# Optimization experiments

Hardware: AMD Instinct MI355X
Metric: run time of the kernel (lower is better)

The kernel has to match this reference:

```python
import jax, jax.numpy as jnp
import numpy as np

HEADS, MAX_SEQ, N_STATE = 8, 2048, 512
DEPTH = N_STATE // HEADS
B, S = 2, 2048
EPS = 1e-5


def setup_inputs() -> dict:
    key = jax.random.key(0)
    ks = jax.random.split(key, 8)
    sd = lambda f: 1.0 / np.sqrt(f)
    causal = jnp.tril(jnp.ones((S, S), dtype=bool))
    mask = jnp.where(causal, 0.0, -1e9).astype(jnp.float32)[None, None]
    return {
        "x": jax.random.normal(ks[0], (B, S, N_STATE), jnp.float32),
        "mask": mask,
        "W_qkv": jax.random.normal(ks[1], (N_STATE, 3 * N_STATE), jnp.float32) * sd(N_STATE),
        "b_qkv": jnp.zeros((3 * N_STATE,), jnp.float32),
        "W_proj": jax.random.normal(ks[2], (N_STATE, N_STATE), jnp.float32) * sd(N_STATE),
        "b_proj": jnp.zeros((N_STATE,), jnp.float32),
        "E": jax.random.normal(ks[3], (HEADS, MAX_SEQ, DEPTH), jnp.float32) * sd(DEPTH),
        "g1": jnp.ones((N_STATE,), jnp.float32),
        "be1": jnp.zeros((N_STATE,), jnp.float32),
        "g2": jnp.ones((N_STATE,), jnp.float32),
        "be2": jnp.zeros((N_STATE,), jnp.float32),
        "W_fc1": jax.random.normal(ks[4], (N_STATE, 4 * N_STATE), jnp.float32) * sd(N_STATE),
        "b_fc1": jnp.zeros((4 * N_STATE,), jnp.float32),
        "W_fc2": jax.random.normal(ks[5], (4 * N_STATE, N_STATE), jnp.float32) * sd(4 * N_STATE),
        "b_fc2": jnp.zeros((N_STATE,), jnp.float32),
    }


def _layernorm(x, g, b):
    mu = jnp.mean(x, axis=-1, keepdims=True)
    var = jnp.mean(jnp.square(x - mu), axis=-1, keepdims=True)
    return (x - mu) * jax.lax.rsqrt(var + EPS) * g + b


def _relative_skew(rel):
    # rel: [B, H, S, S] = q @ E_slice^T ; skew trick -> relative positions
    b, h, s, _ = rel.shape
    rel = jnp.pad(rel, ((0, 0), (0, 0), (0, 0), (1, 0)))  # [B,H,S,S+1]
    rel = rel.reshape(b, h, s + 1, s)
    return rel[:, :, 1:, :]  # [B,H,S,S]


def reference(x, mask, W_qkv, b_qkv, W_proj, b_proj, E, g1, be1, g2, be2,
              W_fc1, b_fc1, W_fc2, b_fc2):
    b, s, _ = x.shape
    a = _layernorm(x, g1, be1)
    qkv = a @ W_qkv + b_qkv  # [B,S,3N]
    q, k, v = jnp.split(qkv, 3, axis=-1)
    split = lambda t: t.reshape(b, s, HEADS, DEPTH).transpose(0, 2, 1, 3)  # [B,H,S,D]
    q, k, v = split(q), split(k), split(v)
    present = jnp.stack([k, v], axis=1)  # [B,2,H,S,D]

    w = jnp.einsum("bhqd,bhkd->bhqk", q, k)
    E_s = E[:, MAX_SEq if False else MAX_SEQ - s:, :]  # [H,S,D]
    rel = jnp.einsum("bhqd,hld->bhql", q, E_s)
    w = (w + _relative_skew(rel)) * (1.0 / np.sqrt(DEPTH))
    w = w + mask
    w = jax.nn.softmax(w, axis=-1)
    att = jnp.einsum("bhqk,bhkd->bhqd", w, v)
    att = att.transpose(0, 2, 1, 3).reshape(b, s, N_STATE)
    att = att @ W_proj + b_proj

    x = x + att
    m = _layernorm(x, g2, be2)
    m = jax.nn.gelu(m @ W_fc1 + b_fc1) @ W_fc2 + b_fc2
    x = x + m
    return (x, present)
```

## Files before the change

### kernel.cpp

```cpp
#include <hip/hip_runtime.h>
#include <stdint.h>

#define DEV __device__ __forceinline__

typedef __attribute__((ext_vector_type(8))) short bf16x8;
typedef __attribute__((ext_vector_type(4))) float f32x4;

DEV ushort f2bf(float f) {
  union { float f; uint32_t u; } c; c.f = f;
  return (ushort)((c.u + 0x7FFFu + ((c.u >> 16) & 1)) >> 16);
}

__global__ __launch_bounds__(256) void k_transpose_bf(const float* __restrict__ in,
                                                      ushort* __restrict__ out,
                                                      int R, int C) {
  __shared__ float t[32][33];
  int tx = threadIdx.x & 31, ty = threadIdx.x >> 5;
  int c0 = blockIdx.x * 32, r0 = blockIdx.y * 32;
#pragma unroll
  for (int k = 0; k < 4; ++k)
    t[ty + 8 * k][tx] = in[(size_t)(r0 + ty + 8 * k) * C + c0 + tx];
  __syncthreads();
#pragma unroll
  for (int k = 0; k < 4; ++k)
    out[(size_t)(c0 + ty + 8 * k) * R + r0 + tx] = f2bf(t[tx][ty + 8 * k]);
}

__global__ __launch_bounds__(256) void k_cvt_bf(const float* __restrict__ in,
                                                ushort* __restrict__ out, int n4) {
  int i = blockIdx.x * 256 + threadIdx.x;
  if (i >= n4) return;
  float4 v = reinterpret_cast<const float4*>(in)[i];
  ushort4 o; o.x = f2bf(v.x); o.y = f2bf(v.y); o.z = f2bf(v.z); o.w = f2bf(v.w);
  reinterpret_cast<ushort4*>(out)[i] = o;
}

__global__ __launch_bounds__(64) void k_ln(const float* __restrict__ x,
                                           const float* __restrict__ g,
                                           const float* __restrict__ be,
                                           ushort* __restrict__ out) {
  int row = blockIdx.x, lane = threadIdx.x;
  const float* xr = x + (size_t)row * 512 + lane * 8;
  float4 a = *reinterpret_cast<const float4*>(xr);
  float4 b = *reinterpret_cast<const float4*>(xr + 4);
  float xs[8] = {a.x, a.y, a.z, a.w, b.x, b.y, b.z, b.w};
  float s = 0.f, q = 0.f;
#pragma unroll
  for (int i = 0; i < 8; ++i) { s += xs[i]; q += xs[i] * xs[i]; }
#pragma unroll
  for (int off = 32; off; off >>= 1) { s += __shfl_xor(s, off); q += __shfl_xor(q, off); }
  float mu = s * (1.f / 512.f);
  float var = q * (1.f / 512.f) - mu * mu;
  float inv = rsqrtf(var + 1e-5f);
  const float* gp = g + lane * 8;
  const float* bp = be + lane * 8;
  ushort o[8];
#pragma unroll
  for (int i = 0; i < 8; ++i) o[i] = f2bf((xs[i] - mu) * inv * gp[i] + bp[i]);
  *reinterpret_cast<uint4*>(out + (size_t)row * 512 + lane * 8) = *reinterpret_cast<uint4*>(o);
}

template <int EPI>
__global__ __launch_bounds__(256) void k_gemm(
    const ushort* __restrict__ A, const ushort* __restrict__ Bt,
    int M, int N, int K,
    const float* __restrict__ bias, const float* __restrict__ res,
    float* __restrict__ outf, ushort* __restrict__ outb,
    float* __restrict__ present, ushort* __restrict__ qbf) {
  __shared__ ushort As[128][72];
  __shared__ ushort Bs[128][72];
  const int tid = threadIdx.x, lane = tid & 63, w = tid >> 6;
  const int g = lane >> 4, l16 = lane & 15;
  const int m0 = blockIdx.y * 128, n0 = blockIdx.x * 128;
  const int wm = (w >> 1) * 64, wn = (w & 1) * 64;
  f32x4 acc[4][4];
#pragma unroll
  for (int i = 0; i < 4; ++i)
#pragma unroll
    for (int j = 0; j < 4; ++j) acc[i][j] = (f32x4){0.f, 0.f, 0.f, 0.f};

  for (int k0 = 0; k0 < K; k0 += 64) {
#pragma unroll
    for (int c = 0; c < 4; ++c) {
      int cc = tid + 256 * c;
      int r = cc >> 3, k8 = (cc & 7) << 3;
      *reinterpret_cast<uint4*>(&As[r][k8]) =
          *reinterpret_cast<const uint4*>(&A[(size_t)(m0 + r) * K + k0 + k8]);
      *reinterpret_cast<uint4*>(&Bs[r][k8]) =
          *reinterpret_cast<const uint4*>(&Bt[(size_t)(n0 + r) * K + k0 + k8]);
    }
    __syncthreads();
#pragma unroll
    for (int kk = 0; kk < 2; ++kk) {
      bf16x8 af[4], bfr[4];
#pragma unroll
      for (int f = 0; f < 4; ++f) {
        af[f] = *reinterpret_cast<const bf16x8*>(&As[wm + f * 16 + l16][kk * 32 + g * 8]);
        bfr[f] = *reinterpret_cast<const bf16x8*>(&Bs[wn + f * 16 + l16][kk * 32 + g * 8]);
      }
#pragma unroll
      for (int i = 0; i < 4; ++i)
#pragma unroll
        for (int j = 0; j < 4; ++j)
          acc[i][j] = __builtin_amdgcn_mfma_f32_16x16x32_bf16(af[i], bfr[j], acc[i][j], 0, 0, 0);
    }
    __syncthreads();
  }

#pragma unroll
  for (int i = 0; i < 4; ++i)
#pragma unroll
    for (int j = 0; j < 4; ++j)
#pragma unroll
      for (int r = 0; r < 4; ++r) {
        int row = m0 + wm + i * 16 + g * 4 + r;
        int col = n0 + wn + j * 16 + l16;
        float v = acc[i][j][r] + bias[col];
        if constexpr (EPI == 0) {
          int third = col >> 9, hh = (col >> 6) & 7, d = col & 63;
          int bb = row >> 11, sq = row & 2047;
          if (third == 0) {
            qbf[((((size_t)bb * 8 + hh) * 2048) + sq) * 64 + d] = f2bf(v);
          } else {
            present[((((size_t)bb * 2 + (third - 1)) * 8 + hh) * 2048 + sq) * 64 + d] = v;
          }
        } else if constexpr (EPI == 1) {
          size_t idx = (size_t)row * N + col;
          outf[idx] = v + res[idx];
        } else {
          float u = 0.7978845608f * (v + 0.044715f * v * v * v);
          float e = __expf(2.f * u);
          float th = 1.f - 2.f / (e + 1.f);
          outb[(size_t)row * N + col] = f2bf(0.5f * v * (1.f + th));
        }
      }
}

__global__ __launch_bounds__(256) void k_attn(
    const ushort* __restrict__ qbf, const float* __restrict__ present,
    const ushort* __restrict__ Ebf, ushort* __restrict__ attb) {
  constexpr int S = 2048;
  __shared__ ushort Ks[64][72];
  __shared__ ushort Vt[64][72];
  __shared__ ushort Es[128][72];
  __shared__ float Rs[4][16][80];
  __shared__ ushort Ps[4][16][72];
  const int tid = threadIdx.x, lane = tid & 63, w = tid >> 6;
  const int g = lane >> 4, l16 = lane & 15;
  const int bh = blockIdx.y, b = bh >> 3, h = bh & 7;
  const float* kp = present + (((size_t)b * 2 + 0) * 8 + h) * S * 64;
  const float* vp = present + (((size_t)b * 2 + 1) * 8 + h) * S * 64;
  const ushort* qp = qbf + (size_t)bh * S * 64;
  const ushort* ep = Ebf + (size_t)h * S * 64;

  for (int half = 0; half < 2; ++half) {
    const int qt = half ? 31 - (int)blockIdx.x : (int)blockIdx.x;
    const int i0 = qt * 64;
    const int iw = i0 + w * 16;
    bf16x8 qf[2];
#pragma unroll
    for (int kk = 0; kk < 2; ++kk)
      qf[kk] = *reinterpret_cast<const bf16x8*>(&qp[(size_t)(iw + l16) * 64 + kk * 32 + g * 8]);
    f32x4 o[4];
#pragma unroll
    for (int fv = 0; fv < 4; ++fv) o[fv] = (f32x4){0.f, 0.f, 0.f, 0.f};
    float mrun[4], lrun[4];
#pragma unroll
    for (int r = 0; r < 4; ++r) { mrun[r] = -1e30f; lrun[r] = 0.f; }

    const int nkt = qt + 1;
    for (int kt = 0; kt < nkt; ++kt) {
      const int j0 = kt * 64;
#pragma unroll
      for (int c = 0; c < 4; ++c) {
        int cc = tid + 256 * c;
        int j = cc >> 4, d4 = (cc & 15) << 2;
        float4 kv = *reinterpret_cast<const float4*>(&kp[(size_t)(j0 + j) * 64 + d4]);
        ushort4 kb; kb.x = f2bf(kv.x); kb.y = f2bf(kv.y); kb.z = f2bf(kv.z); kb.w = f2bf(kv.w);
        *reinterpret_cast<ushort4*>(&Ks[j][d4]) = kb;
        float4 vv = *reinterpret_cast<const float4*>(&vp[(size_t)(j0 + j) * 64 + d4]);
        Vt[d4 + 0][j] = f2bf(vv.x); Vt[d4 + 1][j] = f2bf(vv.y);
        Vt[d4 + 2][j] = f2bf(vv.z); Vt[d4 + 3][j] = f2bf(vv.w);
      }
      const int BS = S - 64 - i0 + j0;
#pragma unroll
      for (int c = 0; c < 4; ++c) {
        int cc = tid + 256 * c;
        int t = cc >> 3, k8 = (cc & 7) << 3;
        int l = BS + t; if (l > S - 1) l = S - 1;
        *reinterpret_cast<uint4*>(&Es[t][k8]) =
            *reinterpret_cast<const uint4*>(&ep[(size_t)l * 64 + k8]);
      }
      __syncthreads();

      f32x4 sacc[4];
#pragma unroll
      for (int fn = 0; fn < 4; ++fn) sacc[fn] = (f32x4){0.f, 0.f, 0.f, 0.f};
#pragma unroll
      for (int kk = 0; kk < 2; ++kk)
#pragma unroll
        for (int fn = 0; fn < 4; ++fn) {
          bf16x8 kf = *reinterpret_cast<const bf16x8*>(&Ks[fn * 16 + l16][kk * 32 + g * 8]);
          sacc[fn] = __builtin_amdgcn_mfma_f32_16x16x32_bf16(qf[kk], kf, sacc[fn], 0, 0, 0);
        }
      const int tb = 48 - 16 * w;
      f32x4 racc[5];
#pragma unroll
      for (int fc = 0; fc < 5; ++fc) racc[fc] = (f32x4){0.f, 0.f, 0.f, 0.f};
#pragma unroll
      for (int kk = 0; kk < 2; ++kk)
#pragma unroll
        for (int fc = 0; fc < 5; ++fc) {
          bf16x8 ef = *reinterpret_cast<const bf16x8*>(&Es[tb + fc * 16 + l16][kk * 32 + g * 8]);
          racc[fc] = __builtin_amdgcn_mfma_f32_16x16x32_bf16(qf[kk], ef, racc[fc], 0, 0, 0);
        }
#pragma unroll
      for (int fc = 0; fc < 5; ++fc)
#pragma unroll
        for (int r = 0; r < 4; ++r)
          Rs[w][g * 4 + r][fc * 16 + l16] = racc[fc][r];

      float Sv[4][4], mtile[4];
#pragma unroll
      for (int r = 0; r < 4; ++r) mtile[r] = -1e30f;
#pragma unroll
      for (int fn = 0; fn < 4; ++fn)
#pragma unroll
        for (int r = 0; r < 4; ++r) {
          int dil = g * 4 + r, dj = fn * 16 + l16;
          float sv = (sacc[fn][r] + Rs[w][dil][15 - dil + dj]) * 0.125f;
          if (j0 + dj > iw + dil) sv = -1e30f;
          Sv[fn][r] = sv;
          mtile[r] = fmaxf(mtile[r], sv);
        }
#pragma unroll
      for (int off = 1; off < 16; off <<= 1)
#pragma unroll
        for (int r = 0; r < 4; ++r) mtile[r] = fmaxf(mtile[r], __shfl_xor(mtile[r], off));
      float corr[4], psum[4];
#pragma unroll
      for (int r = 0; r < 4; ++r) {
        float mn = fmaxf(mrun[r], mtile[r]);
        corr[r] = __expf(mrun[r] - mn);
        mrun[r] = mn;
        psum[r] = 0.f;
      }
#pragma unroll
      for (int fn = 0; fn < 4; ++fn)
#pragma unroll
        for (int r = 0; r < 4; ++r) {
          float p = __expf(Sv[fn][r] - mrun[r]);
          psum[r] += p;
          Ps[w][g * 4 + r][fn * 16 + l16] = f2bf(p);
        }
#pragma unroll
      for (int off = 1; off < 16; off <<= 1)
#pragma unroll
        for (int r = 0; r < 4; ++r) psum[r] += __shfl_xor(psum[r], off);
#pragma unroll
      for (int r = 0; r < 4; ++r) lrun[r] = lrun[r] * corr[r] + psum[r];
#pragma unroll
      for (int fv = 0; fv < 4; ++fv)
#pragma unroll
        for (int r = 0; r < 4; ++r) o[fv][r] *= corr[r];

#pragma unroll
      for (int kk = 0; kk < 2; ++kk) {
        bf16x8 pf = *reinterpret_cast<const bf16x8*>(&Ps[w][l16][kk * 32 + g * 8]);
#pragma unroll
        for (int fv = 0; fv < 4; ++fv) {
          bf16x8 vf = *reinterpret_cast<const bf16x8*>(&Vt[fv * 16 + l16][kk * 32 + g * 8]);
          o[fv] = __builtin_amdgcn_mfma_f32_16x16x32_bf16(pf, vf, o[fv], 0, 0, 0);
        }
      }
      __syncthreads();
    }
#pragma unroll
    for (int fv = 0; fv < 4; ++fv)
#pragma unroll
      for (int r = 0; r < 4; ++r) {
        int dil = g * 4 + r;
        float v = o[fv][r] / lrun[r];
        attb[(size_t)(b * S + iw + dil) * 512 + h * 64 + fv * 16 + l16] = f2bf(v);
      }
  }
}

extern "C" void kernel_launch(void* const* d_in, const int* in_sizes, int n_in,
                              void* d_out, int out_size, void* d_ws, size_t ws_size,
                              hipStream_t stream) {
  const float* x = (const float*)d_in[0];
  const float* W_qkv = (const float*)d_in[2];
  const float* b_qkv = (const float*)d_in[3];
  const float* W_proj = (const float*)d_in[4];
  const float* b_proj = (const float*)d_in[5];
  const float* E = (const float*)d_in[6];
  const float* g1 = (const float*)d_in[7];
  const float* be1 = (const float*)d_in[8];
  const float* g2 = (const float*)d_in[9];
  const float* be2 = (const float*)d_in[10];
  const float* W_fc1 = (const float*)d_in[11];
  const float* b_fc1 = (const float*)d_in[12];
  const float* W_fc2 = (const float*)d_in[13];
  const float* b_fc2 = (const float*)d_in[14];

  float* x_out = (float*)d_out;
  float* present = x_out + 2097152;

  char* ws = (char*)d_ws;
  ushort* a_bf   = (ushort*)(ws + 0);
  ushort* m_bf   = (ushort*)(ws + 4194304);
  ushort* q_bf   = (ushort*)(ws + 8388608);
  ushort* att_bf = (ushort*)(ws + 12582912);
  ushort* h_bf   = (ushort*)(ws + 16777216);
  float*  x2     = (float*)(ws + 33554432);
  ushort* Wqkv_t = (ushort*)(ws + 41943040);
  ushort* Wproj_t= (ushort*)(ws + 43515904);
  ushort* Wfc1_t = (ushort*)(ws + 44040192);
  ushort* Wfc2_t = (ushort*)(ws + 46137344);
  ushort* E_bf   = (ushort*)(ws + 48234496);

  k_transpose_bf<<<dim3(48, 16), 256, 0, stream>>>(W_qkv, Wqkv_t, 512, 1536);
  k_transpose_bf<<<dim3(16, 16), 256, 0, stream>>>(W_proj, Wproj_t, 512, 512);
  k_transpose_bf<<<dim3(64, 16), 256, 0, stream>>>(W_fc1, Wfc1_t, 512, 2048);
  k_transpose_bf<<<dim3(16, 64), 256, 0, stream>>>(W_fc2, Wfc2_t, 2048, 512);
  k_cvt_bf<<<1024, 256, 0, stream>>>(E, E_bf, 262144);
  k_ln<<<4096, 64, 0, stream>>>(x, g1, be1, a_bf);
  k_gemm<0><<<dim3(12, 32), 256, 0, stream>>>(a_bf, Wqkv_t, 4096, 1536, 512,
                                              b_qkv, nullptr, nullptr, nullptr, present, q_bf);
  k_attn<<<dim3(16, 16), 256, 0, stream>>>(q_bf, present, E_bf, att_bf);
  k_gemm<1><<<dim3(4, 32), 256, 0, stream>>>(att_bf, Wproj_t, 4096, 512, 512,
                                             b_proj, x, x2, nullptr, nullptr, nullptr);
  k_ln<<<4096, 64, 0, stream>>>(x2, g2, be2, m_bf);
  k_gemm<2><<<dim3(16, 32), 256, 0, stream>>>(m_bf, Wfc1_t, 4096, 2048, 512,
                                              b_fc1, nullptr, nullptr, h_bf, nullptr, nullptr);
  k_gemm<1><<<dim3(4, 32), 256, 0, stream>>>(h_bf, Wfc2_t, 4096, 512, 2048,
                                             b_fc2, x2, x_out, nullptr, nullptr, nullptr);
}
```

Measured before the change: 299.7 us.

## Restructure attention with split-K waves, bf16 K/Vt from QKV GEMM, LDS-direct GEMM loads

The QKV GEMM epilogue now also writes bf16 K and a transposed bf16 V, so attention no longer converts fp32 present tensors on each tile. The attention kernel is rebuilt as 1024 blocks of two waves. Each block handles 16-row query tiles and splits the key tiles between its two waves, which merge their online-softmax states through LDS at the end. K, V and E fragments are now read directly from global memory instead of being staged in shared memory. Separately, the GEMM now loads tiles with global_load_lds into unpadded LDS, which may cause bank conflicts and drops any K/V reuse from shared staging.

```diff
diff --git a/kernel.cpp b/kernel.cpp
--- a/kernel.cpp
+++ b/kernel.cpp
@@ -9,6 +9,13 @@
 DEV ushort f2bf(float f) {
   union { float f; uint32_t u; } c; c.f = f;
   return (ushort)((c.u + 0x7FFFu + ((c.u >> 16) & 1)) >> 16);
+}
+DEV bf16x8 ld8(const ushort* p) { return *reinterpret_cast<const bf16x8*>(p); }
+
+DEV void gload16(const void* g, void* l) {
+  __builtin_amdgcn_global_load_lds(
+      (const __attribute__((address_space(1))) uint32_t*)g,
+      (__attribute__((address_space(3))) uint32_t*)l, 16, 0, 0);
 }
 
 __global__ __launch_bounds__(256) void k_transpose_bf(const float* __restrict__ in,
@@ -66,9 +73,10 @@
     int M, int N, int K,
     const float* __restrict__ bias, const float* __restrict__ res,
     float* __restrict__ outf, ushort* __restrict__ outb,
-    float* __restrict__ present, ushort* __restrict__ qbf) {
-  __shared__ ushort As[128][72];
-  __shared__ ushort Bs[128][72];
+    float* __restrict__ present, ushort* __restrict__ qbf,
+    ushort* __restrict__ kbf, ushort* __restrict__ vtbf) {
+  __shared__ ushort As[128][64];
+  __shared__ ushort Bs[128][64];
   const int tid = threadIdx.x, lane = tid & 63, w = tid >> 6;
   const int g = lane >> 4, l16 = lane & 15;
   const int m0 = blockIdx.y * 128, n0 = blockIdx.x * 128;
@@ -79,15 +87,17 @@
 #pragma unroll
     for (int j = 0; j < 4; ++j) acc[i][j] = (f32x4){0.f, 0.f, 0.f, 0.f};
 
+  const int lrow_off = (lane << 4);
   for (int k0 = 0; k0 < K; k0 += 64) {
 #pragma unroll
-    for (int c = 0; c < 4; ++c) {
-      int cc = tid + 256 * c;
-      int r = cc >> 3, k8 = (cc & 7) << 3;
-      *reinterpret_cast<uint4*>(&As[r][k8]) =
-          *reinterpret_cast<const uint4*>(&A[(size_t)(m0 + r) * K + k0 + k8]);
-      *reinterpret_cast<uint4*>(&Bs[r][k8]) =
-          *reinterpret_cast<const uint4*>(&Bt[(size_t)(n0 + r) * K + k0 + k8]);
+    for (int sw = 0; sw < 4; ++sw) {
+      int offb = sw * 4096 + w * 1024;
+      int loff = offb + lrow_off;
+      int row = loff >> 7, colb = loff & 127;
+      gload16((const char*)A + (((size_t)(m0 + row) * K + k0) << 1) + colb,
+              (char*)As + offb);
+      gload16((const char*)Bt + (((size_t)(n0 + row) * K + k0) << 1) + colb,
+              (char*)Bs + offb);
     }
     __syncthreads();
 #pragma unroll
@@ -123,6 +133,10 @@
             qbf[((((size_t)bb * 8 + hh) * 2048) + sq) * 64 + d] = f2bf(v);
           } else {
             present[((((size_t)bb * 2 + (third - 1)) * 8 + hh) * 2048 + sq) * 64 + d] = v;
+            if (third == 1)
+              kbf[((((size_t)bb * 8 + hh) * 2048) + sq) * 64 + d] = f2bf(v);
+            else
+              vtbf[(((size_t)bb * 8 + hh) * 64 + d) * 2048 + sq] = f2bf(v);
           }
         } else if constexpr (EPI == 1) {
           size_t idx = (size_t)row * N + col;
@@ -136,63 +150,41 @@
       }
 }
 
-__global__ __launch_bounds__(256) void k_attn(
-    const ushort* __restrict__ qbf, const float* __restrict__ present,
-    const ushort* __restrict__ Ebf, ushort* __restrict__ attb) {
+__global__ __launch_bounds__(128) void k_attn(
+    const ushort* __restrict__ qbf, const ushort* __restrict__ kbf,
+    const ushort* __restrict__ vtbf, const ushort* __restrict__ Ebf,
+    ushort* __restrict__ attb) {
   constexpr int S = 2048;
-  __shared__ ushort Ks[64][72];
-  __shared__ ushort Vt[64][72];
-  __shared__ ushort Es[128][72];
-  __shared__ float Rs[4][16][80];
-  __shared__ ushort Ps[4][16][72];
-  const int tid = threadIdx.x, lane = tid & 63, w = tid >> 6;
+  __shared__ float Rs[2][16][84];
+  __shared__ ushort Ps[2][16][76];
+  __shared__ float Mrg[2][64][24];
+  const int tid = threadIdx.x, lane = tid & 63, ks = tid >> 6;
   const int g = lane >> 4, l16 = lane & 15;
-  const int bh = blockIdx.y, b = bh >> 3, h = bh & 7;
-  const float* kp = present + (((size_t)b * 2 + 0) * 8 + h) * S * 64;
-  const float* vp = present + (((size_t)b * 2 + 1) * 8 + h) * S * 64;
+  const int bid = blockIdx.x;
+  const int xcd = bid & 7, idx = bid >> 3;
+  const int b = idx & 1, p = idx >> 1;
+  const int h = xcd, bh = b * 8 + h;
   const ushort* qp = qbf + (size_t)bh * S * 64;
+  const ushort* kp = kbf + (size_t)bh * S * 64;
+  const ushort* vp = vtbf + (size_t)bh * 64 * S;
   const ushort* ep = Ebf + (size_t)h * S * 64;
 
-  for (int half = 0; half < 2; ++half) {
-    const int qt = half ? 31 - (int)blockIdx.x : (int)blockIdx.x;
-    const int i0 = qt * 64;
-    const int iw = i0 + w * 16;
+  for (int si = 0; si < 2; ++si) {
+    const int t = si ? (127 - p) : p;
+    const int i0 = t * 16;
     bf16x8 qf[2];
-#pragma unroll
-    for (int kk = 0; kk < 2; ++kk)
-      qf[kk] = *reinterpret_cast<const bf16x8*>(&qp[(size_t)(iw + l16) * 64 + kk * 32 + g * 8]);
+    qf[0] = ld8(qp + (size_t)(i0 + l16) * 64 + g * 8);
+    qf[1] = ld8(qp + (size_t)(i0 + l16) * 64 + 32 + g * 8);
     f32x4 o[4];
 #pragma unroll
     for (int fv = 0; fv < 4; ++fv) o[fv] = (f32x4){0.f, 0.f, 0.f, 0.f};
     float mrun[4], lrun[4];
 #pragma unroll
     for (int r = 0; r < 4; ++r) { mrun[r] = -1e30f; lrun[r] = 0.f; }
-
-    const int nkt = qt + 1;
-    for (int kt = 0; kt < nkt; ++kt) {
+    const int nkt = t / 4 + 1;
+
+    for (int kt = ks; kt < nkt; kt += 2) {
       const int j0 = kt * 64;
-#pragma unroll
-      for (int c = 0; c < 4; ++c) {
-        int cc = tid + 256 * c;
-        int j = cc >> 4, d4 = (cc & 15) << 2;
-        float4 kv = *reinterpret_cast<const float4*>(&kp[(size_t)(j0 + j) * 64 + d4]);
-        ushort4 kb; kb.x = f2bf(kv.x); kb.y = f2bf(kv.y); kb.z = f2bf(kv.z); kb.w = f2bf(kv.w);
-        *reinterpret_cast<ushort4*>(&Ks[j][d4]) = kb;
-        float4 vv = *reinterpret_cast<const float4*>(&vp[(size_t)(j0 + j) * 64 + d4]);
-        Vt[d4 + 0][j] = f2bf(vv.x); Vt[d4 + 1][j] = f2bf(vv.y);
-        Vt[d4 + 2][j] = f2bf(vv.z); Vt[d4 + 3][j] = f2bf(vv.w);
-      }
-      const int BS = S - 64 - i0 + j0;
-#pragma unroll
-      for (int c = 0; c < 4; ++c) {
-        int cc = tid + 256 * c;
-        int t = cc >> 3, k8 = (cc & 7) << 3;
-        int l = BS + t; if (l > S - 1) l = S - 1;
-        *reinterpret_cast<uint4*>(&Es[t][k8]) =
-            *reinterpret_cast<const uint4*>(&ep[(size_t)l * 64 + k8]);
-      }
-      __syncthreads();
-
       f32x4 sacc[4];
 #pragma unroll
       for (int fn = 0; fn < 4; ++fn) sacc[fn] = (f32x4){0.f, 0.f, 0.f, 0.f};
@@ -200,10 +192,10 @@
       for (int kk = 0; kk < 2; ++kk)
 #pragma unroll
         for (int fn = 0; fn < 4; ++fn) {
-          bf16x8 kf = *reinterpret_cast<const bf16x8*>(&Ks[fn * 16 + l16][kk * 32 + g * 8]);
+          bf16x8 kf = ld8(kp + (size_t)(j0 + fn * 16 + l16) * 64 + kk * 32 + g * 8);
           sacc[fn] = __builtin_amdgcn_mfma_f32_16x16x32_bf16(qf[kk], kf, sacc[fn], 0, 0, 0);
         }
-      const int tb = 48 - 16 * w;
+      const int tb = S - 16 - i0 + j0;
       f32x4 racc[5];
 #pragma unroll
       for (int fc = 0; fc < 5; ++fc) racc[fc] = (f32x4){0.f, 0.f, 0.f, 0.f};
@@ -211,14 +203,15 @@
       for (int kk = 0; kk < 2; ++kk)
 #pragma unroll
         for (int fc = 0; fc < 5; ++fc) {
-          bf16x8 ef = *reinterpret_cast<const bf16x8*>(&Es[tb + fc * 16 + l16][kk * 32 + g * 8]);
+          int l = tb + fc * 16 + l16; if (l > S - 1) l = S - 1;
+          bf16x8 ef = ld8(ep + (size_t)l * 64 + kk * 32 + g * 8);
           racc[fc] = __builtin_amdgcn_mfma_f32_16x16x32_bf16(qf[kk], ef, racc[fc], 0, 0, 0);
         }
 #pragma unroll
       for (int fc = 0; fc < 5; ++fc)
 #pragma unroll
         for (int r = 0; r < 4; ++r)
-          Rs[w][g * 4 + r][fc * 16 + l16] = racc[fc][r];
+          Rs[ks][g * 4 + r][fc * 16 + l16] = racc[fc][r];
 
       float Sv[4][4], mtile[4];
 #pragma unroll
@@ -227,9 +220,9 @@
       for (int fn = 0; fn < 4; ++fn)
 #pragma unroll
         for (int r = 0; r < 4; ++r) {
-          int dil = g * 4 + r, dj = fn * 16 + l16;
-          float sv = (sacc[fn][r] + Rs[w][dil][15 - dil + dj]) * 0.125f;
-          if (j0 + dj > iw + dil) sv = -1e30f;
+          int dr = g * 4 + r, dj = fn * 16 + l16;
+          float sv = (sacc[fn][r] + Rs[ks][dr][15 - dr + dj]) * 0.125f;
+          if (j0 + dj > i0 + dr) sv = -1e30f;
           Sv[fn][r] = sv;
           mtile[r] = fmaxf(mtile[r], sv);
         }
@@ -249,9 +242,9 @@
       for (int fn = 0; fn < 4; ++fn)
 #pragma unroll
         for (int r = 0; r < 4; ++r) {
-          float p = __expf(Sv[fn][r] - mrun[r]);
-          psum[r] += p;
-          Ps[w][g * 4 + r][fn * 16 + l16] = f2bf(p);
+          float pv = __expf(Sv[fn][r] - mrun[r]);
+          psum[r] += pv;
+          Ps[ks][g * 4 + r][fn * 16 + l16] = f2bf(pv);
         }
 #pragma unroll
       for (int off = 1; off < 16; off <<= 1)
@@ -266,23 +259,42 @@
 
 #pragma unroll
       for (int kk = 0; kk < 2; ++kk) {
-        bf16x8 pf = *reinterpret_cast<const bf16x8*>(&Ps[w][l16][kk * 32 + g * 8]);
+        bf16x8 pf = ld8(&Ps[ks][l16][kk * 32 + g * 8]);
 #pragma unroll
         for (int fv = 0; fv < 4; ++fv) {
-          bf16x8 vf = *reinterpret_cast<const bf16x8*>(&Vt[fv * 16 + l16][kk * 32 + g * 8]);
+          bf16x8 vf = ld8(vp + (size_t)(fv * 16 + l16) * S + j0 + kk * 32 + g * 8);
           o[fv] = __builtin_amdgcn_mfma_f32_16x16x32_bf16(pf, vf, o[fv], 0, 0, 0);
         }
       }
-      __syncthreads();
-    }
-#pragma unroll
-    for (int fv = 0; fv < 4; ++fv)
+    }
+
+    if (ks == 1) {
+      float* mb = &Mrg[si][lane][0];
+#pragma unroll
+      for (int fv = 0; fv < 4; ++fv)
+#pragma unroll
+        for (int r = 0; r < 4; ++r) mb[fv * 4 + r] = o[fv][r];
+#pragma unroll
+      for (int r = 0; r < 4; ++r) { mb[16 + r] = mrun[r]; mb[20 + r] = lrun[r]; }
+    }
+    __syncthreads();
+    if (ks == 0) {
+      const float* mb = &Mrg[si][lane][0];
 #pragma unroll
       for (int r = 0; r < 4; ++r) {
-        int dil = g * 4 + r;
-        float v = o[fv][r] / lrun[r];
-        attb[(size_t)(b * S + iw + dil) * 512 + h * 64 + fv * 16 + l16] = f2bf(v);
-      }
+        float m1 = mb[16 + r];
+        float mm = fmaxf(mrun[r], m1);
+        float e0 = __expf(mrun[r] - mm), e1 = __expf(m1 - mm);
+        float lc = lrun[r] * e0 + mb[20 + r] * e1;
+        float inv = 1.f / lc;
+#pragma unroll
+        for (int fv = 0; fv < 4; ++fv) {
+          float oc = o[fv][r] * e0 + mb[fv * 4 + r] * e1;
+          attb[(size_t)(b * S + i0 + g * 4 + r) * 512 + h * 64 + fv * 16 + l16] =
+              f2bf(oc * inv);
+        }
+      }
+    }
   }
 }
 
@@ -313,6 +325,8 @@
   ushort* q_bf   = (ushort*)(ws + 8388608);
   ushort* att_bf = (ushort*)(ws + 12582912);
   ushort* h_bf   = (ushort*)(ws + 16777216);
+  ushort* k_bf   = (ushort*)(ws + 16777216);
+  ushort* vt_bf  = (ushort*)(ws + 20971520);
   float*  x2     = (float*)(ws + 33554432);
   ushort* Wqkv_t = (ushort*)(ws + 41943040);
   ushort* Wproj_t= (ushort*)(ws + 43515904);
@@ -327,13 +341,17 @@
   k_cvt_bf<<<1024, 256, 0, stream>>>(E, E_bf, 262144);
   k_ln<<<4096, 64, 0, stream>>>(x, g1, be1, a_bf);
   k_gemm<0><<<dim3(12, 32), 256, 0, stream>>>(a_bf, Wqkv_t, 4096, 1536, 512,
-                                              b_qkv, nullptr, nullptr, nullptr, present, q_bf);
-  k_attn<<<dim3(16, 16), 256, 0, stream>>>(q_bf, present, E_bf, att_bf);
+                                              b_qkv, nullptr, nullptr, nullptr,
+                                              present, q_bf, k_bf, vt_bf);
+  k_attn<<<1024, 128, 0, stream>>>(q_bf, k_bf, vt_bf, E_bf, att_bf);
   k_gemm<1><<<dim3(4, 32), 256, 0, stream>>>(att_bf, Wproj_t, 4096, 512, 512,
-                                             b_proj, x, x2, nullptr, nullptr, nullptr);
+                                             b_proj, x, x2, nullptr, nullptr, nullptr,
+                                             nullptr, nullptr);
   k_ln<<<4096, 64, 0, stream>>>(x2, g2, be2, m_bf);
   k_gemm<2><<<dim3(16, 32), 256, 0, stream>>>(m_bf, Wfc1_t, 4096, 2048, 512,
-                                              b_fc1, nullptr, nullptr, h_bf, nullptr, nullptr);
+                                              b_fc1, nullptr, nullptr, h_bf, nullptr,
+                                              nullptr, nullptr, nullptr);
   k_gemm<1><<<dim3(4, 32), 256, 0, stream>>>(h_bf, Wfc2_t, 4096, 512, 2048,
-                                             b_fc2, x2, x_out, nullptr, nullptr, nullptr);
-}
+                                             b_fc2, x2, x_out, nullptr, nullptr, nullptr,
+                                             nullptr, nullptr);
+}
```

Result: slower. 336.1 us (+12.2%).
